# Kernel tuning notes

Measured on AMD Instinct MI355X. Metric: run time of the kernel, lower is better.

The kernel has to match this reference:

```python
import jax, jax.numpy as jnp
import numpy as np

B, S, E = 2, 2048, 1024
INNER = 2048          # proj_factor * embedding_dim
NH = 4                # mLSTM heads
K = 4                 # causal conv kernel size
PH, PD = 512, 4       # headwise-proj heads (inner/qkv_proj_blocksize) and block size


def setup_inputs() -> dict:
    key = jax.random.key(0)
    ks = jax.random.split(key, 10)
    f = lambda k, shape, s=0.02: jax.random.normal(k, shape, jnp.float32) * s
    return dict(
        x=jax.random.normal(ks[0], (B, S, E), jnp.float32),
        W_up=f(ks[1], (E, 2 * INNER)),
        conv_w=f(ks[2], (K, INNER), 0.1),
        conv_b=jnp.zeros((INNER,), jnp.float32),
        Wq=f(ks[3], (PH, PD, PD), 0.3),
        Wk=f(ks[4], (PH, PD, PD), 0.3),
        Wv=f(ks[5], (PH, PD, PD), 0.3),
        W_ig=f(ks[6], (3 * INNER, NH), 0.01),
        b_ig=jnp.zeros((NH,), jnp.float32),
        W_fg=f(ks[7], (3 * INNER, NH), 0.01),
        b_fg=jnp.linspace(3.0, 6.0, NH).astype(jnp.float32),
        norm_w=jnp.ones((INNER,), jnp.float32),
        skip=jnp.ones((INNER,), jnp.float32),
        W_down=f(ks[8], (INNER, E)),
    )


def _forward(x, W_up, conv_w, conv_b, Wq, Wk, Wv, W_ig, b_ig, W_fg, b_fg,
             norm_w, skip, W_down):
    Bx, Sx, _ = x.shape
    # up projection then split into mlstm branch and gate branch z
    x_inner = x @ W_up                                  # (B,S,2*INNER)
    x_mlstm, z = jnp.split(x_inner, 2, axis=-1)
    # causal depthwise conv1d (left-pad K-1)
    Kk = conv_w.shape[0]
    x_pad = jnp.pad(x_mlstm, ((0, 0), (Kk - 1, 0), (0, 0)))
    x_conv = sum(x_pad[:, i:i + Sx, :] * conv_w[i] for i in range(Kk)) + conv_b
    x_act = jax.nn.swish(x_conv)

    def headwise(t, W):
        H, o, d = W.shape
        return jnp.einsum('bshd,hod->bsho', t.reshape(Bx, Sx, H, d), W).reshape(Bx, Sx, H * o)

    q = headwise(x_act, Wq)
    k = headwise(x_act, Wk)
    v = headwise(x_mlstm, Wv)
    Dm = q.shape[-1]
    NHn = b_ig.shape[0]
    DH = Dm // NHn
    qh = q.reshape(Bx, Sx, NHn, DH).transpose(0, 2, 1, 3)   # (B,NH,S,DH)
    kh = k.reshape(Bx, Sx, NHn, DH).transpose(0, 2, 1, 3)
    vh = v.reshape(Bx, Sx, NHn, DH).transpose(0, 2, 1, 3)
    # input / forget gate preactivations from concat(q,k,v)
    if_in = jnp.concatenate([q, k, v], axis=-1)             # (B,S,3*INNER)
    ig = (if_in @ W_ig + b_ig).transpose(0, 2, 1)[..., None]  # (B,NH,S,1)
    fg = (if_in @ W_fg + b_fg).transpose(0, 2, 1)[..., None]
    # parallel stabilized mLSTM (matrix memory, exp gating)
    log_f = jax.nn.log_sigmoid(fg)
    lfc = jnp.concatenate([jnp.zeros((Bx, NHn, 1, 1), log_f.dtype),
                           jnp.cumsum(log_f, axis=2)], axis=2)  # (B,NH,S+1,1)
    lfm = lfc - jnp.swapaxes(lfc, -2, -1)                   # (B,NH,S+1,S+1)
    mask = jnp.tril(jnp.ones((Sx + 1, Sx + 1), bool))
    lfm = jnp.where(mask, lfm, -jnp.inf)[:, :, 1:, 1:]      # (B,NH,S,S)
    logD = lfm + jnp.swapaxes(ig, -2, -1)
    mD = jnp.max(logD, axis=-1, keepdims=True)
    Dmat = jnp.exp(logD - mD)
    C = jnp.einsum('bnsd,bntd->bnst', qh, kh) * (DH ** -0.5) * Dmat
    norm = jnp.maximum(jnp.abs(C.sum(-1, keepdims=True)), jnp.exp(-mD))
    h = jnp.einsum('bnst,bntd->bnsd', C / (norm + 1e-6), vh)  # (B,NH,S,DH)
    # multi-head layernorm over DH, then merge heads
    mu = h.mean(-1, keepdims=True)
    var = ((h - mu) ** 2).mean(-1, keepdims=True)
    hn = ((h - mu) * jax.lax.rsqrt(var + 1e-6)).transpose(0, 2, 1, 3).reshape(Bx, Sx, Dm)
    hn = hn * norm_w
    # learnable skip from conv activation, gate with swish(z), down proj
    h_state = (hn + skip * x_act) * jax.nn.swish(z)
    return h_state @ W_down


def reference(x, W_up, conv_w, conv_b, Wq, Wk, Wv, W_ig, b_ig, W_fg, b_fg,
              norm_w, skip, W_down):
    return _forward(x, W_up, conv_w, conv_b, Wq, Wk, Wv, W_ig, b_ig, W_fg,
                    b_fg, norm_w, skip, W_down)
```

## Files before the change

### kernel.cpp

```cpp
#include <hip/hip_runtime.h>
#include <math.h>

#define S_LEN 2048
#define INNERD 2048
#define NHEAD 4
#define DHEAD 512
#define BATCH 2
#define SCALE_QK 0.044194173824159216f

typedef __attribute__((ext_vector_type(8))) short short8v;
typedef __attribute__((ext_vector_type(4))) float f32x4;

#define MFMA_BF16(A, B, C) __builtin_amdgcn_mfma_f32_16x16x32_bf16(A, B, C, 0, 0, 0)

__device__ __forceinline__ void gll16(const void* g, void* l) {
  __builtin_amdgcn_global_load_lds((const __attribute__((address_space(1))) unsigned int*)g,
                                   (__attribute__((address_space(3))) unsigned int*)l,
                                   16, 0, 0);
}

__device__ __forceinline__ unsigned short f2bf(float x) {
  union { float f; unsigned u; } v; v.f = x;
  unsigned r = v.u + 0x7FFFu + ((v.u >> 16) & 1u);
  return (unsigned short)(r >> 16);
}
__device__ __forceinline__ float bf2f(unsigned short x) {
  union { unsigned u; float f; } v; v.u = ((unsigned)x) << 16; return v.f;
}
__device__ __forceinline__ float swishf(float x) { return x / (1.0f + __expf(-x)); }
__device__ __forceinline__ float logsigf(float x) {
  return (x >= 0.0f) ? -log1pf(expf(-x)) : (x - log1pf(expf(x)));
}

__global__ __launch_bounds__(256) void cast_kernel(const float* __restrict__ src,
                                                   unsigned short* __restrict__ dst) {
  const int i = (blockIdx.x * 256 + threadIdx.x) * 8;
  const float4 a = *(const float4*)(src + i);
  const float4 b = *(const float4*)(src + i + 4);
  short8v o;
  o[0] = (short)f2bf(a.x); o[1] = (short)f2bf(a.y); o[2] = (short)f2bf(a.z); o[3] = (short)f2bf(a.w);
  o[4] = (short)f2bf(b.x); o[5] = (short)f2bf(b.y); o[6] = (short)f2bf(b.z); o[7] = (short)f2bf(b.w);
  *(short8v*)(dst + i) = o;
}

__global__ __launch_bounds__(256) void trc_kernel(const float* __restrict__ src,
                                                  unsigned short* __restrict__ dst,
                                                  int R, int C) {
  const int t = threadIdx.x;
  const int r0 = blockIdx.y * 128, c0 = blockIdx.x * 128;
  const int rb = (t >> 4) * 8, cb2 = (t & 15) * 8;
  float vreg[8][8];
#pragma unroll
  for (int u = 0; u < 8; ++u) {
    const float4 p0 = *(const float4*)(src + (size_t)(r0 + rb + u) * C + c0 + cb2);
    const float4 p1 = *(const float4*)(src + (size_t)(r0 + rb + u) * C + c0 + cb2 + 4);
    vreg[u][0] = p0.x; vreg[u][1] = p0.y; vreg[u][2] = p0.z; vreg[u][3] = p0.w;
    vreg[u][4] = p1.x; vreg[u][5] = p1.y; vreg[u][6] = p1.z; vreg[u][7] = p1.w;
  }
#pragma unroll
  for (int j = 0; j < 8; ++j) {
    short8v o;
#pragma unroll
    for (int u = 0; u < 8; ++u) o[u] = (short)f2bf(vreg[u][j]);
    *(short8v*)(dst + (size_t)(c0 + cb2 + j) * R + r0 + rb) = o;
  }
}

__global__ __launch_bounds__(256) void trv_kernel(const unsigned short* __restrict__ v,
                                                  unsigned short* __restrict__ vt) {
  const int t = threadIdx.x;
  const int s0 = blockIdx.x * 128;
  const int d0 = blockIdx.y * 128;
  const int bn = blockIdx.z;
  const int b = bn >> 2, n = bn & 3;
  const int sb = (t >> 4) * 8, db = (t & 15) * 8;
  unsigned short r[8][8];
#pragma unroll
  for (int u = 0; u < 8; ++u) {
    const short8v x2 = *(const short8v*)(v + (size_t)(b * S_LEN + s0 + sb + u) * INNERD + n * DHEAD + d0 + db);
#pragma unroll
    for (int j = 0; j < 8; ++j) r[u][j] = (unsigned short)x2[j];
  }
#pragma unroll
  for (int j = 0; j < 8; ++j) {
    short8v o;
#pragma unroll
    for (int u = 0; u < 8; ++u) o[u] = (short)r[u][j];
    *(short8v*)(vt + (size_t)(bn * DHEAD + d0 + db + j) * S_LEN + s0 + sb) = o;
  }
}

__global__ __launch_bounds__(256) void prep_kernel(
    const float* __restrict__ Wq, const float* __restrict__ Wk, const float* __restrict__ Wv,
    const float* __restrict__ Wig, const float* __restrict__ Wfg,
    unsigned short* __restrict__ Wpk, unsigned short* __restrict__ CgT) {
  const int t = threadIdx.x;
  float wq[2][16], wk[2][16], wv[2][16];
#pragma unroll
  for (int hh = 0; hh < 2; ++hh) {
    const int h = 2 * t + hh;
#pragma unroll
    for (int j = 0; j < 16; ++j) {
      wq[hh][j] = Wq[(size_t)h * 16 + j];
      wk[hh][j] = Wk[(size_t)h * 16 + j];
      wv[hh][j] = Wv[(size_t)h * 16 + j];
    }
  }
#pragma unroll
  for (int hh = 0; hh < 2; ++hh)
#pragma unroll
    for (int sub = 0; sub < 2; ++sub) {
      short8v oq, ok, ov;
#pragma unroll
      for (int j = 0; j < 8; ++j) {
        oq[j] = (short)f2bf(wq[hh][sub * 8 + j]);
        ok[j] = (short)f2bf(wk[hh][sub * 8 + j]);
        ov[j] = (short)f2bf(wv[hh][sub * 8 + j]);
      }
      *(short8v*)(Wpk + ((size_t)(0 + hh * 2 + sub) * 256 + t) * 8) = oq;
      *(short8v*)(Wpk + ((size_t)(4 + hh * 2 + sub) * 256 + t) * 8) = ok;
      *(short8v*)(Wpk + ((size_t)(8 + hh * 2 + sub) * 256 + t) * 8) = ov;
    }
#pragma unroll
  for (int u = 0; u < 8; ++u) {
    const int hh = u >> 2, d = u & 3;
    const int h = 2 * t + hh;
    float cia[4] = {0, 0, 0, 0}, cim[4] = {0, 0, 0, 0};
    float cfa[4] = {0, 0, 0, 0}, cfm[4] = {0, 0, 0, 0};
#pragma unroll
    for (int o = 0; o < 4; ++o) {
      const int row = h * 4 + o;
      const float aq = wq[hh][o * 4 + d], ak = wk[hh][o * 4 + d], av = wv[hh][o * 4 + d];
#pragma unroll
      for (int g = 0; g < 4; ++g) {
        cia[g] += aq * Wig[(size_t)row * 4 + g] + ak * Wig[(size_t)(INNERD + row) * 4 + g];
        cim[g] += av * Wig[(size_t)(2 * INNERD + row) * 4 + g];
        cfa[g] += aq * Wfg[(size_t)row * 4 + g] + ak * Wfg[(size_t)(INNERD + row) * 4 + g];
        cfm[g] += av * Wfg[(size_t)(2 * INNERD + row) * 4 + g];
      }
    }
    const int c = t * 8 + u;
#pragma unroll
    for (int g = 0; g < 4; ++g) {
      CgT[(size_t)(g) * INNERD + c] = f2bf(cia[g]);
      CgT[(size_t)(4 + g) * INNERD + c] = f2bf(cim[g]);
      CgT[(size_t)(8 + g) * INNERD + c] = f2bf(cfa[g]);
      CgT[(size_t)(12 + g) * INNERD + c] = f2bf(cfm[g]);
    }
  }
}

template <int BN, int OUTMODE>
__global__ __launch_bounds__(256) void gemm_bf16(const unsigned short* __restrict__ A,
                                                 const unsigned short* __restrict__ Bt,
                                                 float* __restrict__ Cf,
                                                 unsigned short* __restrict__ Cb0,
                                                 unsigned short* __restrict__ Cb1,
                                                 int M, int N, int K) {
  constexpr int CB = BN / 32;
  __shared__ unsigned short As[128 * 64];
  __shared__ unsigned short Bs[BN * 64];
  const int tid = threadIdx.x;
  const int w = tid >> 6, l = tid & 63;
  const int lm = l & 15, l4 = l >> 4, l8 = l & 7, lr = l >> 3;
  const int nwg = gridDim.x * gridDim.y;
  int bid = blockIdx.y * gridDim.x + blockIdx.x;
  const int cpx = nwg >> 3;
  bid = (bid & 7) * cpx + (bid >> 3);
  const int bx = bid % gridDim.x, by = bid / gridDim.x;
  const int row0 = by * 128, col0 = bx * BN;
  const int wm = w >> 1, wn = w & 1;
  f32x4 acc[4 * CB];
#pragma unroll
  for (int i2 = 0; i2 < 4 * CB; ++i2) acc[i2] = (f32x4){0.f, 0.f, 0.f, 0.f};

  const int scol = (l8 * 16) ^ (lr << 4);

  for (int k0 = 0; k0 < K; k0 += 64) {
#pragma unroll
    for (int it = 0; it < 4; ++it) {
      const int r = it * 32 + w * 8 + lr;
      gll16((const char*)A + ((size_t)(row0 + r) * K + k0) * 2 + scol,
            (char*)As + (size_t)(it * 32 + w * 8) * 128);
    }
#pragma unroll
    for (int it = 0; it < BN / 32; ++it) {
      const int r = it * 32 + w * 8 + lr;
      gll16((const char*)Bt + ((size_t)(col0 + r) * K + k0) * 2 + scol,
            (char*)Bs + (size_t)(it * 32 + w * 8) * 128);
    }
    __syncthreads();
#pragma unroll
    for (int ks = 0; ks < 2; ++ks) {
      short8v af[4], bfr[CB];
#pragma unroll
      for (int rb = 0; rb < 4; ++rb) {
        const int row = wm * 64 + rb * 16 + lm;
        af[rb] = *(const short8v*)((const char*)As + row * 128 + ((ks * 64 + l4 * 16) ^ ((lm & 7) << 4)));
      }
#pragma unroll
      for (int cb = 0; cb < CB; ++cb) {
        const int row = wn * (BN / 2) + cb * 16 + lm;
        bfr[cb] = *(const short8v*)((const char*)Bs + row * 128 + ((ks * 64 + l4 * 16) ^ ((lm & 7) << 4)));
      }
      __builtin_amdgcn_s_setprio(1);
#pragma unroll
      for (int rb = 0; rb < 4; ++rb)
#pragma unroll
        for (int cb = 0; cb < CB; ++cb)
          acc[rb * CB + cb] = MFMA_BF16(af[rb], bfr[cb], acc[rb * CB + cb]);
      __builtin_amdgcn_s_setprio(0);
    }
    __syncthreads();
  }
#pragma unroll
  for (int rb = 0; rb < 4; ++rb)
#pragma unroll
    for (int cb = 0; cb < CB; ++cb)
#pragma unroll
      for (int r = 0; r < 4; ++r) {
        const int gr = row0 + wm * 64 + rb * 16 + l4 * 4 + r;
        const int gc = col0 + wn * (BN / 2) + cb * 16 + lm;
        const float vv = acc[rb * CB + cb][r];
        if (OUTMODE == 0) {
          Cf[(size_t)gr * N + gc] = vv;
        } else {
          if (gc < 2048) Cb0[(size_t)gr * 2048 + gc] = f2bf(vv);
          else Cb1[(size_t)gr * 2048 + gc - 2048] = f2bf(vv);
        }
      }
}

__global__ __launch_bounds__(256) void headwise_kernel(
    const unsigned short* __restrict__ xm,
    const unsigned short* __restrict__ Wpk, const unsigned short* __restrict__ CgT,
    const float* __restrict__ cw, const float* __restrict__ cbias,
    const float* __restrict__ big, const float* __restrict__ bfg,
    unsigned short* __restrict__ q, unsigned short* __restrict__ k,
    unsigned short* __restrict__ v,
    float* __restrict__ igpre, float* __restrict__ fgpre) {
  __shared__ float red2[4][8];
  const int bs = blockIdx.x, t = threadIdx.x;
  const int s = bs & (S_LEN - 1);
  const int c0 = t * 8;
  float xa8[8], xm8[8];
  {
    float accv[8];
    const float4 cb0 = *(const float4*)(cbias + c0);
    const float4 cb1 = *(const float4*)(cbias + c0 + 4);
    accv[0] = cb0.x; accv[1] = cb0.y; accv[2] = cb0.z; accv[3] = cb0.w;
    accv[4] = cb1.x; accv[5] = cb1.y; accv[6] = cb1.z; accv[7] = cb1.w;
#pragma unroll
    for (int i = 0; i < 4; ++i) {
      if (s - 3 + i >= 0) {
        const short8v xv = *(const short8v*)(xm + (size_t)(bs - 3 + i) * INNERD + c0);
        const float4 w0 = *(const float4*)(cw + i * INNERD + c0);
        const float4 w1 = *(const float4*)(cw + i * INNERD + c0 + 4);
        const float wv2[8] = {w0.x, w0.y, w0.z, w0.w, w1.x, w1.y, w1.z, w1.w};
#pragma unroll
        for (int u = 0; u < 8; ++u) accv[u] += bf2f((unsigned short)xv[u]) * wv2[u];
      }
    }
    const short8v xs = *(const short8v*)(xm + (size_t)bs * INNERD + c0);
#pragma unroll
    for (int u = 0; u < 8; ++u) { xm8[u] = bf2f((unsigned short)xs[u]); xa8[u] = swishf(accv[u]); }
  }
  short8v qo, ko, vo;
#pragma unroll
  for (int hh = 0; hh < 2; ++hh)
#pragma unroll
    for (int sub = 0; sub < 2; ++sub) {
      const short8v wq = *(const short8v*)(Wpk + ((size_t)(0 + hh * 2 + sub) * 256 + t) * 8);
      const short8v wk = *(const short8v*)(Wpk + ((size_t)(4 + hh * 2 + sub) * 256 + t) * 8);
      const short8v wv3 = *(const short8v*)(Wpk + ((size_t)(8 + hh * 2 + sub) * 256 + t) * 8);
      float ql = 0, qh = 0, kl = 0, kh2 = 0, vl = 0, vh = 0;
#pragma unroll
      for (int d = 0; d < 4; ++d) {
        const float xa = xa8[hh * 4 + d], xv2 = xm8[hh * 4 + d];
        ql += bf2f((unsigned short)wq[d]) * xa;
        qh += bf2f((unsigned short)wq[4 + d]) * xa;
        kl += bf2f((unsigned short)wk[d]) * xa;
        kh2 += bf2f((unsigned short)wk[4 + d]) * xa;
        vl += bf2f((unsigned short)wv3[d]) * xv2;
        vh += bf2f((unsigned short)wv3[4 + d]) * xv2;
      }
      qo[hh * 4 + sub * 2] = (short)f2bf(ql); qo[hh * 4 + sub * 2 + 1] = (short)f2bf(qh);
      ko[hh * 4 + sub * 2] = (short)f2bf(kl); ko[hh * 4 + sub * 2 + 1] = (short)f2bf(kh2);
      vo[hh * 4 + sub * 2] = (short)f2bf(vl); vo[hh * 4 + sub * 2 + 1] = (short)f2bf(vh);
    }
  *(short8v*)(q + (size_t)bs * INNERD + c0) = qo;
  *(short8v*)(k + (size_t)bs * INNERD + c0) = ko;
  *(short8v*)(v + (size_t)bs * INNERD + c0) = vo;
  float r8[8];
#pragma unroll
  for (int j = 0; j < 4; ++j) {
    const short8v ca = *(const short8v*)(CgT + (size_t)j * INNERD + c0);
    const short8v cm = *(const short8v*)(CgT + (size_t)(4 + j) * INNERD + c0);
    const short8v fa = *(const short8v*)(CgT + (size_t)(8 + j) * INNERD + c0);
    const short8v fm = *(const short8v*)(CgT + (size_t)(12 + j) * INNERD + c0);
    float si = 0.f, sf = 0.f;
#pragma unroll
    for (int u = 0; u < 8; ++u) {
      si += xa8[u] * bf2f((unsigned short)ca[u]) + xm8[u] * bf2f((unsigned short)cm[u]);
      sf += xa8[u] * bf2f((unsigned short)fa[u]) + xm8[u] * bf2f((unsigned short)fm[u]);
    }
    r8[j] = si; r8[4 + j] = sf;
  }
  const int l = t & 63;
  const bool b1 = (l & 1), b2 = (l & 2), b4 = (l & 4);
  float t4[4];
#pragma unroll
  for (int i = 0; i < 4; ++i) {
    const float send = b1 ? r8[i] : r8[i + 4];
    const float recv = __shfl_xor(send, 1, 64);
    t4[i] = (b1 ? r8[i + 4] : r8[i]) + recv;
  }
  float u2[2];
#pragma unroll
  for (int i = 0; i < 2; ++i) {
    const float send = b2 ? t4[i] : t4[i + 2];
    const float recv = __shfl_xor(send, 2, 64);
    u2[i] = (b2 ? t4[i + 2] : t4[i]) + recv;
  }
  float wsum;
  {
    const float send = b4 ? u2[0] : u2[1];
    const float recv = __shfl_xor(send, 4, 64);
    wsum = (b4 ? u2[1] : u2[0]) + recv;
  }
  wsum += __shfl_xor(wsum, 8, 64);
  wsum += __shfl_xor(wsum, 16, 64);
  wsum += __shfl_xor(wsum, 32, 64);
  if (l < 8) {
    const int perm = ((l & 1) << 2) | (l & 2) | ((l >> 2) & 1);
    red2[t >> 6][perm] = wsum;
  }
  __syncthreads();
  if (t < 8) {
    const float sum = red2[0][t] + red2[1][t] + red2[2][t] + red2[3][t];
    const int b = bs >> 11;
    if (t < 4) igpre[((size_t)(b * NHEAD + t)) * S_LEN + s] = sum + big[t];
    else fgpre[((size_t)(b * NHEAD + t - 4)) * S_LEN + s] = sum + bfg[t - 4];
  }
}

__global__ __launch_bounds__(256) void scan_kernel(const float* __restrict__ igpre,
                                                   const float* __restrict__ fgpre,
                                                   float* __restrict__ a_o,
                                                   float* __restrict__ rm_o,
                                                   float* __restrict__ e_o) {
  __shared__ float sd[256];
  const int bn = blockIdx.x, t = threadIdx.x;
  const size_t base = (size_t)bn * S_LEN + t * 8;
  float cs[8];
  float run = 0.0f;
#pragma unroll
  for (int u = 0; u < 8; ++u) { run += logsigf(fgpre[base + u]); cs[u] = run; }
  sd[t] = run;
  __syncthreads();
  for (int off = 1; off < 256; off <<= 1) {
    const float vv2 = (t >= off) ? sd[t - off] : 0.0f;
    __syncthreads();
    sd[t] += vv2;
    __syncthreads();
  }
  const float exs = (t > 0) ? sd[t - 1] : 0.0f;
  __syncthreads();
  float av[8], pm[8];
  float rmax = -INFINITY;
#pragma unroll
  for (int u = 0; u < 8; ++u) {
    const float L = exs + cs[u];
    cs[u] = L;
    av[u] = igpre[base + u] - L;
    rmax = fmaxf(rmax, av[u]);
    pm[u] = rmax;
  }
  sd[t] = rmax;
  __syncthreads();
  for (int off = 1; off < 256; off <<= 1) {
    const float vv2 = (t >= off) ? sd[t - off] : -INFINITY;
    __syncthreads();
    sd[t] = fmaxf(sd[t], vv2);
    __syncthreads();
  }
  const float exm = (t > 0) ? sd[t - 1] : -INFINITY;
#pragma unroll
  for (int u = 0; u < 8; ++u) {
    const float rmv = fmaxf(exm, pm[u]);
    a_o[base + u] = av[u];
    rm_o[base + u] = rmv;
    e_o[base + u] = expf(-(cs[u] + rmv));
  }
}

__global__ __launch_bounds__(512, 2) void mlstm_mfma(
    const unsigned short* __restrict__ qg, const unsigned short* __restrict__ kg,
    const unsigned short* __restrict__ vtg,
    const float* __restrict__ ag, const float* __restrict__ rmg,
    float* __restrict__ hraw, float* __restrict__ rsumg) {
  __shared__ unsigned short Ks[2][64 * 512];
  __shared__ unsigned short Ps[64 * 64];
  __shared__ float rsl[8][16];
  const int tid = threadIdx.x;
  const int w = tid >> 6, l = tid & 63;
  const int lm = l & 15, l4 = l >> 4;
  const int beta = blockIdx.x;
  const int bn = beta & 7;
  const int part = (beta >> 3) & 1;
  const int idx = beta >> 4;
  const int qi = (idx < 16) ? (31 - idx) : (idx - 16);
  const int i0 = qi << 6;
  const int b = bn >> 2, n = bn & 3;
  float* hp = hraw + (size_t)part * ((size_t)BATCH * S_LEN * INNERD);
  float* rp = rsumg + (size_t)part * ((size_t)BATCH * NHEAD * S_LEN);

  const int rA = ((w >> 1) << 4) + lm;
  short8v qf[16];
  {
    const unsigned short* qp = qg + (size_t)(b * S_LEN + i0 + rA) * INNERD + n * DHEAD + l4 * 8;
#pragma unroll
    for (int ks = 0; ks < 16; ++ks) qf[ks] = *(const short8v*)(qp + ks * 32);
  }
  const int rD = ((w >> 1) << 4) + (l4 << 2);
  float rm4[4];
#pragma unroll
  for (int r = 0; r < 4; ++r) rm4[r] = rmg[(size_t)bn * S_LEN + i0 + rD + r];
  const int cb0 = (w & 1) << 1;

  f32x4 acc[16];
#pragma unroll
  for (int i2 = 0; i2 < 16; ++i2) acc[i2] = (f32x4){0.f, 0.f, 0.f, 0.f};
  float rs4[4] = {0.f, 0.f, 0.f, 0.f};

  const int ntau = (qi + 2 - part) >> 1;
  __builtin_amdgcn_sched_barrier(0);
  if (ntau > 0) {
#pragma unroll
    for (int it = 0; it < 8; ++it) {
      const int row = it * 8 + w;
      gll16((const char*)kg + ((size_t)(b * S_LEN + part * 64 + row) * INNERD + n * DHEAD) * 2 + ((l * 16) ^ (w << 4)),
            (char*)Ks[0] + row * 1024);
    }
  }
  __builtin_amdgcn_sched_barrier(0);

  for (int tau = 0; tau < ntau; ++tau) {
    const int j0 = (part + 2 * tau) << 6;
    const int cur = tau & 1;
    short8v vf[8];
#pragma unroll
    for (int db = 0; db < 4; ++db)
#pragma unroll
      for (int ks = 0; ks < 2; ++ks)
        vf[db * 2 + ks] = *(const short8v*)(vtg + (size_t)(bn * DHEAD + w * 64 + db * 16 + lm) * S_LEN + j0 + ks * 32 + l4 * 8);
    const float a0 = ag[(size_t)bn * S_LEN + j0 + cb0 * 16 + lm];
    const float a1 = ag[(size_t)bn * S_LEN + j0 + cb0 * 16 + 16 + lm];
    __builtin_amdgcn_sched_barrier(0);
    const bool hasnext = (tau + 1 < ntau);
    if (hasnext) {
#pragma unroll
      for (int it = 0; it < 8; ++it) {
        const int row = it * 8 + w;
        gll16((const char*)kg + ((size_t)(b * S_LEN + j0 + 128 + row) * INNERD + n * DHEAD) * 2 + ((l * 16) ^ (w << 4)),
              (char*)Ks[cur ^ 1] + row * 1024);
      }
    }
    __builtin_amdgcn_sched_barrier(0);
    if (hasnext) { asm volatile("s_waitcnt vmcnt(18)" ::: "memory"); }
    else         { asm volatile("s_waitcnt vmcnt(10)" ::: "memory"); }
    __builtin_amdgcn_sched_barrier(0);
    __builtin_amdgcn_s_barrier();
    f32x4 s0 = (f32x4){0.f, 0.f, 0.f, 0.f}, s1 = (f32x4){0.f, 0.f, 0.f, 0.f};
    const char* kb0 = (const char*)Ks[cur] + (cb0 * 16 + lm) * 1024;
    const char* kb1 = (const char*)Ks[cur] + ((cb0 + 1) * 16 + lm) * 1024;
    __builtin_amdgcn_s_setprio(1);
#pragma unroll
    for (int ks = 0; ks < 16; ++ks) {
      const int off = (ks * 64 + l4 * 16) ^ ((lm & 7) << 4);
      const short8v b0 = *(const short8v*)(kb0 + off);
      const short8v b1 = *(const short8v*)(kb1 + off);
      s0 = MFMA_BF16(qf[ks], b0, s0);
      s1 = MFMA_BF16(qf[ks], b1, s1);
    }
    __builtin_amdgcn_s_setprio(0);
#pragma unroll
    for (int half = 0; half < 2; ++half) {
      const f32x4 sv = half ? s1 : s0;
      const float av = half ? a1 : a0;
      const int jl = (cb0 + half) * 16 + lm;
#pragma unroll
      for (int r = 0; r < 4; ++r) {
        const int il = rD + r;
        const float es = __expf(av - rm4[r]);
        const float p = (j0 + jl <= i0 + il) ? sv[r] * SCALE_QK * es : 0.0f;
        rs4[r] += p;
        *((unsigned short*)((char*)Ps + il * 128 + ((jl * 2) ^ ((il & 7) << 4)))) = f2bf(p);
      }
    }
    asm volatile("s_waitcnt lgkmcnt(0)" ::: "memory");
    __builtin_amdgcn_sched_barrier(0);
    __builtin_amdgcn_s_barrier();
#pragma unroll
    for (int ks = 0; ks < 2; ++ks) {
      short8v pa[4];
#pragma unroll
      for (int rb = 0; rb < 4; ++rb)
        pa[rb] = *(const short8v*)((const char*)Ps + (rb * 16 + lm) * 128 + ((ks * 64 + l4 * 16) ^ ((lm & 7) << 4)));
      __builtin_amdgcn_s_setprio(1);
#pragma unroll
      for (int rb = 0; rb < 4; ++rb)
#pragma unroll
        for (int db = 0; db < 4; ++db)
          acc[rb * 4 + db] = MFMA_BF16(pa[rb], vf[db * 2 + ks], acc[rb * 4 + db]);
      __builtin_amdgcn_s_setprio(0);
    }
  }
#pragma unroll
  for (int r = 0; r < 4; ++r) {
    float v2 = rs4[r];
    v2 += __shfl_xor(v2, 1, 64);
    v2 += __shfl_xor(v2, 2, 64);
    v2 += __shfl_xor(v2, 4, 64);
    v2 += __shfl_xor(v2, 8, 64);
    if (lm == 0) rsl[w][l4 * 4 + r] = v2;
  }
  asm volatile("s_waitcnt lgkmcnt(0)" ::: "memory");
  __builtin_amdgcn_s_barrier();
  if (tid < 64) {
    const int rblk = tid >> 4, rloc = tid & 15;
    rp[(size_t)bn * S_LEN + i0 + rblk * 16 + rloc] = rsl[rblk * 2][rloc] + rsl[rblk * 2 + 1][rloc];
  }
#pragma unroll
  for (int rb = 0; rb < 4; ++rb)
#pragma unroll
    for (int db = 0; db < 4; ++db) {
      float* dst = hp + (size_t)(b * S_LEN + i0 + rb * 16 + l4 * 4) * INNERD + n * DHEAD + w * 64 + db * 16 + lm;
#pragma unroll
      for (int r = 0; r < 4; ++r) dst[(size_t)r * INNERD] = acc[rb * 4 + db][r];
    }
}

__global__ __launch_bounds__(256) void mhln_kernel(
    const float* __restrict__ h, const unsigned short* __restrict__ xm,
    const unsigned short* __restrict__ zb,
    const float* __restrict__ cw, const float* __restrict__ cbias,
    const float* __restrict__ rsumg, const float* __restrict__ eg,
    const float* __restrict__ normw, const float* __restrict__ skip,
    unsigned short* __restrict__ hstate) {
  const int bs = blockIdx.x, t = threadIdx.x;
  const int bb = bs >> 11, s = bs & (S_LEN - 1);
  const int n = t >> 6, lane = t & 63;
  const int cp0 = n * DHEAD + lane * 8;
  const size_t hb = (size_t)bs * INNERD + cp0;
  const size_t HOFF = (size_t)BATCH * S_LEN * INNERD;
  const int bn = bb * NHEAD + n;
  const float rsv = rsumg[(size_t)bn * S_LEN + s] + rsumg[(size_t)BATCH * NHEAD * S_LEN + bn * S_LEN + s];
  const float ev = eg[(size_t)bn * S_LEN + s];
  const float inorm = 1.0f / (fmaxf(fabsf(rsv), ev) + 1e-6f);
  const float4 v0 = *(const float4*)(h + hb);
  const float4 v1 = *(const float4*)(h + hb + 4);
  const float4 u0 = *(const float4*)(h + HOFF + hb);
  const float4 u1 = *(const float4*)(h + HOFF + hb + 4);
  float vals[8] = {(v0.x + u0.x) * inorm, (v0.y + u0.y) * inorm, (v0.z + u0.z) * inorm,
                   (v0.w + u0.w) * inorm, (v1.x + u1.x) * inorm, (v1.y + u1.y) * inorm,
                   (v1.z + u1.z) * inorm, (v1.w + u1.w) * inorm};
  float sum = 0.0f;
#pragma unroll
  for (int u = 0; u < 8; ++u) sum += vals[u];
#pragma unroll
  for (int m = 32; m >= 1; m >>= 1) sum += __shfl_xor(sum, m, 64);
  const float mu = sum * (1.0f / 512.0f);
  float vs2 = 0.0f;
#pragma unroll
  for (int u = 0; u < 8; ++u) { const float d = vals[u] - mu; vs2 += d * d; }
#pragma unroll
  for (int m = 32; m >= 1; m >>= 1) vs2 += __shfl_xor(vs2, m, 64);
  const float rstd = rsqrtf(vs2 * (1.0f / 512.0f) + 1e-6f);
  float xa8[8];
  {
    float accv[8];
#pragma unroll
    for (int u = 0; u < 8; ++u) accv[u] = cbias[cp0 + u];
#pragma unroll
    for (int i2 = 0; i2 < 4; ++i2) {
      const int sj = s - 3 + i2;
      if (sj >= 0) {
        const short8v xv = *(const short8v*)(xm + (size_t)(bs - 3 + i2) * INNERD + cp0);
#pragma unroll
        for (int u = 0; u < 8; ++u)
          accv[u] += bf2f((unsigned short)xv[u]) * cw[i2 * INNERD + cp0 + u];
      }
    }
#pragma unroll
    for (int u = 0; u < 8; ++u) xa8[u] = swishf(accv[u]);
  }
  const short8v zv = *(const short8v*)(zb + (size_t)bs * INNERD + cp0);
  short8v o;
#pragma unroll
  for (int u = 0; u < 8; ++u) {
    const int cp = cp0 + u;
    const float hn = (vals[u] - mu) * rstd * normw[cp];
    const float z = bf2f((unsigned short)zv[u]);
    o[u] = (short)f2bf((hn + skip[cp] * xa8[u]) * swishf(z));
  }
  *(short8v*)(hstate + hb) = o;
}

extern "C" void kernel_launch(void* const* d_in, const int* in_sizes, int n_in,
                              void* d_out, int out_size, void* d_ws, size_t ws_size,
                              hipStream_t stream) {
  const float* x     = (const float*)d_in[0];
  const float* Wup   = (const float*)d_in[1];
  const float* cw    = (const float*)d_in[2];
  const float* cb    = (const float*)d_in[3];
  const float* Wq    = (const float*)d_in[4];
  const float* Wk    = (const float*)d_in[5];
  const float* Wv    = (const float*)d_in[6];
  const float* Wig   = (const float*)d_in[7];
  const float* big   = (const float*)d_in[8];
  const float* Wfg   = (const float*)d_in[9];
  const float* bfg   = (const float*)d_in[10];
  const float* normw = (const float*)d_in[11];
  const float* skip  = (const float*)d_in[12];
  const float* Wdown = (const float*)d_in[13];
  float* out = (float*)d_out;

  float* ws = (float*)d_ws;
  size_t off = 0;
  const size_t MR = (size_t)BATCH * S_LEN;
  const size_t GSZ = (size_t)BATCH * NHEAD * S_LEN;
  unsigned short* xm  = (unsigned short*)(ws + off); off += MR * INNERD / 2;
  unsigned short* zb  = (unsigned short*)(ws + off); off += MR * INNERD / 2;
  float* hraw         = ws + off;                    off += 2 * MR * INNERD;
  unsigned short* qb  = (unsigned short*)(ws + off); off += MR * INNERD / 2;
  unsigned short* kb  = (unsigned short*)(ws + off); off += MR * INNERD / 2;
  unsigned short* vt  = (unsigned short*)(ws + off); off += MR * INNERD / 2;
  float* igpre  = ws + off; off += GSZ;
  float* fgpre  = ws + off; off += GSZ;
  float* a_buf  = ws + off; off += GSZ;
  float* rm_buf = ws + off; off += GSZ;
  float* e_buf  = ws + off; off += GSZ;
  float* rsum   = ws + off; off += 2 * GSZ;
  unsigned short* Wpk = (unsigned short*)(ws + off); off += 12 * 256 * 8 / 2;
  unsigned short* CgT = (unsigned short*)(ws + off); off += 16 * (size_t)INNERD / 2;
  if (ws_size < off * sizeof(float)) return;

  unsigned short* vb     = (unsigned short*)hraw;
  unsigned short* x_bf   = (unsigned short*)(hraw + MR * INNERD);
  unsigned short* WupT   = vt;
  unsigned short* WdT    = kb;
  unsigned short* hstate = qb;

  prep_kernel<<<1, 256, 0, stream>>>(Wq, Wk, Wv, Wig, Wfg, Wpk, CgT);
  cast_kernel<<<2048, 256, 0, stream>>>(x, x_bf);
  trc_kernel<<<dim3(32, 8), 256, 0, stream>>>(Wup, WupT, 1024, 4096);
  gemm_bf16<128, 1><<<dim3(32, 32), 256, 0, stream>>>(x_bf, WupT, nullptr, xm, zb, 4096, 4096, 1024);
  headwise_kernel<<<4096, 256, 0, stream>>>(xm, Wpk, CgT, cw, cb, big, bfg,
                                            qb, kb, vb, igpre, fgpre);
  trv_kernel<<<dim3(16, 4, 8), 256, 0, stream>>>(vb, vt);
  scan_kernel<<<8, 256, 0, stream>>>(igpre, fgpre, a_buf, rm_buf, e_buf);
  mlstm_mfma<<<512, 512, 0, stream>>>(qb, kb, vt, a_buf, rm_buf, hraw, rsum);
  trc_kernel<<<dim3(8, 16), 256, 0, stream>>>(Wdown, WdT, 2048, 1024);
  mhln_kernel<<<4096, 256, 0, stream>>>(hraw, xm, zb, cw, cb, rsum, e_buf, normw, skip, hstate);
  gemm_bf16<64, 0><<<dim3(16, 32), 256, 0, stream>>>(hstate, WdT, out, nullptr, nullptr, 4096, 1024, 2048);
}
```

Measured before the change: 396.2 us.

## Read K fragments directly from global memory instead of LDS double buffer

Removes the double-buffered 128KB LDS staging of K tiles (async global-to-LDS loads, vmcnt waits and a per-iteration barrier), and has each wave load its K fragments straight from global/L2 into registers for the QK MFMA. The P tile is double-buffered in LDS so the first per-iteration barrier can be dropped without a write-after-read hazard. This cuts LDS use sharply, which may raise occupancy and remove sync, but each wave now issues uncoalesced 16-byte global loads with no prefetch, so latency is exposed and K data is re-read by multiple waves.

Measured after the change: 525.2 us. 1.33x slower.

```diff
diff --git a/kernel.cpp b/kernel.cpp
--- a/kernel.cpp
+++ b/kernel.cpp
@@ -399,8 +399,7 @@
     const unsigned short* __restrict__ vtg,
     const float* __restrict__ ag, const float* __restrict__ rmg,
     float* __restrict__ hraw, float* __restrict__ rsumg) {
-  __shared__ unsigned short Ks[2][64 * 512];
-  __shared__ unsigned short Ps[64 * 64];
+  __shared__ unsigned short Ps[2][64 * 64];
   __shared__ float rsl[8][16];
   const int tid = threadIdx.x;
   const int w = tid >> 6, l = tid & 63;
@@ -428,23 +427,15 @@
   for (int r = 0; r < 4; ++r) rm4[r] = rmg[(size_t)bn * S_LEN + i0 + rD + r];
   const int cb0 = (w & 1) << 1;
 
+  const unsigned short* kb0 = kg + (size_t)(b * S_LEN + cb0 * 16 + lm) * INNERD + n * DHEAD + l4 * 8;
+  const unsigned short* kb1 = kb0 + (size_t)16 * INNERD;
+
   f32x4 acc[16];
 #pragma unroll
   for (int i2 = 0; i2 < 16; ++i2) acc[i2] = (f32x4){0.f, 0.f, 0.f, 0.f};
   float rs4[4] = {0.f, 0.f, 0.f, 0.f};
 
   const int ntau = (qi + 2 - part) >> 1;
-  __builtin_amdgcn_sched_barrier(0);
-  if (ntau > 0) {
-#pragma unroll
-    for (int it = 0; it < 8; ++it) {
-      const int row = it * 8 + w;
-      gll16((const char*)kg + ((size_t)(b * S_LEN + part * 64 + row) * INNERD + n * DHEAD) * 2 + ((l * 16) ^ (w << 4)),
-            (char*)Ks[0] + row * 1024);
-    }
-  }
-  __builtin_amdgcn_sched_barrier(0);
-
   for (int tau = 0; tau < ntau; ++tau) {
     const int j0 = (part + 2 * tau) << 6;
     const int cur = tau & 1;
@@ -456,34 +447,16 @@
         vf[db * 2 + ks] = *(const short8v*)(vtg + (size_t)(bn * DHEAD + w * 64 + db * 16 + lm) * S_LEN + j0 + ks * 32 + l4 * 8);
     const float a0 = ag[(size_t)bn * S_LEN + j0 + cb0 * 16 + lm];
     const float a1 = ag[(size_t)bn * S_LEN + j0 + cb0 * 16 + 16 + lm];
-    __builtin_amdgcn_sched_barrier(0);
-    const bool hasnext = (tau + 1 < ntau);
-    if (hasnext) {
-#pragma unroll
-      for (int it = 0; it < 8; ++it) {
-        const int row = it * 8 + w;
-        gll16((const char*)kg + ((size_t)(b * S_LEN + j0 + 128 + row) * INNERD + n * DHEAD) * 2 + ((l * 16) ^ (w << 4)),
-              (char*)Ks[cur ^ 1] + row * 1024);
-      }
-    }
-    __builtin_amdgcn_sched_barrier(0);
-    if (hasnext) { asm volatile("s_waitcnt vmcnt(18)" ::: "memory"); }
-    else         { asm volatile("s_waitcnt vmcnt(10)" ::: "memory"); }
-    __builtin_amdgcn_sched_barrier(0);
-    __builtin_amdgcn_s_barrier();
+    const unsigned short* kp0 = kb0 + (size_t)j0 * INNERD;
+    const unsigned short* kp1 = kb1 + (size_t)j0 * INNERD;
     f32x4 s0 = (f32x4){0.f, 0.f, 0.f, 0.f}, s1 = (f32x4){0.f, 0.f, 0.f, 0.f};
-    const char* kb0 = (const char*)Ks[cur] + (cb0 * 16 + lm) * 1024;
-    const char* kb1 = (const char*)Ks[cur] + ((cb0 + 1) * 16 + lm) * 1024;
-    __builtin_amdgcn_s_setprio(1);
 #pragma unroll
     for (int ks = 0; ks < 16; ++ks) {
-      const int off = (ks * 64 + l4 * 16) ^ ((lm & 7) << 4);
-      const short8v b0 = *(const short8v*)(kb0 + off);
-      const short8v b1 = *(const short8v*)(kb1 + off);
-      s0 = MFMA_BF16(qf[ks], b0, s0);
-      s1 = MFMA_BF16(qf[ks], b1, s1);
-    }
-    __builtin_amdgcn_s_setprio(0);
+      const short8v k0 = *(const short8v*)(kp0 + ks * 32);
+      const short8v k1 = *(const short8v*)(kp1 + ks * 32);
+      s0 = MFMA_BF16(qf[ks], k0, s0);
+      s1 = MFMA_BF16(qf[ks], k1, s1);
+    }
 #pragma unroll
     for (int half = 0; half < 2; ++half) {
       const f32x4 sv = half ? s1 : s0;
@@ -495,7 +468,7 @@
         const float es = __expf(av - rm4[r]);
         const float p = (j0 + jl <= i0 + il) ? sv[r] * SCALE_QK * es : 0.0f;
         rs4[r] += p;
-        *((unsigned short*)((char*)Ps + il * 128 + ((jl * 2) ^ ((il & 7) << 4)))) = f2bf(p);
+        *((unsigned short*)((char*)Ps[cur] + il * 128 + ((jl * 2) ^ ((il & 7) << 4)))) = f2bf(p);
       }
     }
     asm volatile("s_waitcnt lgkmcnt(0)" ::: "memory");
@@ -506,7 +479,7 @@
       short8v pa[4];
 #pragma unroll
       for (int rb = 0; rb < 4; ++rb)
-        pa[rb] = *(const short8v*)((const char*)Ps + (rb * 16 + lm) * 128 + ((ks * 64 + l4 * 16) ^ ((lm & 7) << 4)));
+        pa[rb] = *(const short8v*)((const char*)Ps[cur] + (rb * 16 + lm) * 128 + ((ks * 64 + l4 * 16) ^ ((lm & 7) << 4)));
       __builtin_amdgcn_s_setprio(1);
 #pragma unroll
       for (int rb = 0; rb < 4; ++rb)
```

## Fuse setup kernels into one launch and store mLSTM partials as bf16

Applied to the files above, without the earlier changes.

Merges the input cast, both weight transposes and the gate-weight prep into a single setup kernel, removing several launches and moving the W_down transpose earlier. The mLSTM kernel now writes its two partial outputs in bf16 instead of fp32, halving write and read traffic into the layernorm kernel. It also removes the priority hints around the MFMA loop in the GEMM. The bf16 partials lose some precision before normalization, and workspace aliasing is reorganized.

After: 382.1 us. -3.5%, faster.

```diff
diff --git a/kernel.cpp b/kernel.cpp
--- a/kernel.cpp
+++ b/kernel.cpp
@@ -32,22 +32,9 @@
   return (x >= 0.0f) ? -log1pf(expf(-x)) : (x - log1pf(expf(x)));
 }
 
-__global__ __launch_bounds__(256) void cast_kernel(const float* __restrict__ src,
-                                                   unsigned short* __restrict__ dst) {
-  const int i = (blockIdx.x * 256 + threadIdx.x) * 8;
-  const float4 a = *(const float4*)(src + i);
-  const float4 b = *(const float4*)(src + i + 4);
-  short8v o;
-  o[0] = (short)f2bf(a.x); o[1] = (short)f2bf(a.y); o[2] = (short)f2bf(a.z); o[3] = (short)f2bf(a.w);
-  o[4] = (short)f2bf(b.x); o[5] = (short)f2bf(b.y); o[6] = (short)f2bf(b.z); o[7] = (short)f2bf(b.w);
-  *(short8v*)(dst + i) = o;
-}
-
-__global__ __launch_bounds__(256) void trc_kernel(const float* __restrict__ src,
-                                                  unsigned short* __restrict__ dst,
-                                                  int R, int C) {
-  const int t = threadIdx.x;
-  const int r0 = blockIdx.y * 128, c0 = blockIdx.x * 128;
+__device__ __forceinline__ void trc_body(const float* __restrict__ src,
+                                         unsigned short* __restrict__ dst,
+                                         int R, int C, int r0, int c0, int t) {
   const int rb = (t >> 4) * 8, cb2 = (t & 15) * 8;
   float vreg[8][8];
 #pragma unroll
@@ -63,6 +50,87 @@
 #pragma unroll
     for (int u = 0; u < 8; ++u) o[u] = (short)f2bf(vreg[u][j]);
     *(short8v*)(dst + (size_t)(c0 + cb2 + j) * R + r0 + rb) = o;
+  }
+}
+
+__global__ __launch_bounds__(256) void setup_kernel(
+    const float* __restrict__ x, const float* __restrict__ Wup,
+    const float* __restrict__ Wdown,
+    const float* __restrict__ Wq, const float* __restrict__ Wk, const float* __restrict__ Wv,
+    const float* __restrict__ Wig, const float* __restrict__ Wfg,
+    unsigned short* __restrict__ x_bf, unsigned short* __restrict__ WupT,
+    unsigned short* __restrict__ WdT,
+    unsigned short* __restrict__ Wpk, unsigned short* __restrict__ CgT) {
+  const int bid = blockIdx.x;
+  const int t = threadIdx.x;
+  if (bid < 2048) {
+    const int i = (bid * 256 + t) * 8;
+    const float4 a = *(const float4*)(x + i);
+    const float4 b = *(const float4*)(x + i + 4);
+    short8v o;
+    o[0] = (short)f2bf(a.x); o[1] = (short)f2bf(a.y); o[2] = (short)f2bf(a.z); o[3] = (short)f2bf(a.w);
+    o[4] = (short)f2bf(b.x); o[5] = (short)f2bf(b.y); o[6] = (short)f2bf(b.z); o[7] = (short)f2bf(b.w);
+    *(short8v*)(x_bf + i) = o;
+  } else if (bid < 2304) {
+    const int local = bid - 2048;
+    trc_body(Wup, WupT, 1024, 4096, (local >> 5) * 128, (local & 31) * 128, t);
+  } else if (bid < 2432) {
+    const int local = bid - 2304;
+    trc_body(Wdown, WdT, 2048, 1024, (local >> 3) * 128, (local & 7) * 128, t);
+  } else {
+    float wq[2][16], wk[2][16], wv[2][16];
+#pragma unroll
+    for (int hh = 0; hh < 2; ++hh) {
+      const int h = 2 * t + hh;
+#pragma unroll
+      for (int j = 0; j < 16; ++j) {
+        wq[hh][j] = Wq[(size_t)h * 16 + j];
+        wk[hh][j] = Wk[(size_t)h * 16 + j];
+        wv[hh][j] = Wv[(size_t)h * 16 + j];
+      }
+    }
+#pragma unroll
+    for (int hh = 0; hh < 2; ++hh)
+#pragma unroll
+      for (int sub = 0; sub < 2; ++sub) {
+        short8v oq, ok, ov;
+#pragma unroll
+        for (int j = 0; j < 8; ++j) {
+          oq[j] = (short)f2bf(wq[hh][sub * 8 + j]);
+          ok[j] = (short)f2bf(wk[hh][sub * 8 + j]);
+          ov[j] = (short)f2bf(wv[hh][sub * 8 + j]);
+        }
+        *(short8v*)(Wpk + ((size_t)(0 + hh * 2 + sub) * 256 + t) * 8) = oq;
+        *(short8v*)(Wpk + ((size_t)(4 + hh * 2 + sub) * 256 + t) * 8) = ok;
+        *(short8v*)(Wpk + ((size_t)(8 + hh * 2 + sub) * 256 + t) * 8) = ov;
+      }
+#pragma unroll
+    for (int u = 0; u < 8; ++u) {
+      const int hh = u >> 2, d = u & 3;
+      const int h = 2 * t + hh;
+      float cia[4] = {0, 0, 0, 0}, cim[4] = {0, 0, 0, 0};
+      float cfa[4] = {0, 0, 0, 0}, cfm[4] = {0, 0, 0, 0};
+#pragma unroll
+      for (int o = 0; o < 4; ++o) {
+        const int row = h * 4 + o;
+        const float aq = wq[hh][o * 4 + d], ak = wk[hh][o * 4 + d], av = wv[hh][o * 4 + d];
+#pragma unroll
+        for (int g = 0; g < 4; ++g) {
+          cia[g] += aq * Wig[(size_t)row * 4 + g] + ak * Wig[(size_t)(INNERD + row) * 4 + g];
+          cim[g] += av * Wig[(size_t)(2 * INNERD + row) * 4 + g];
+          cfa[g] += aq * Wfg[(size_t)row * 4 + g] + ak * Wfg[(size_t)(INNERD + row) * 4 + g];
+          cfm[g] += av * Wfg[(size_t)(2 * INNERD + row) * 4 + g];
+        }
+      }
+      const int c = t * 8 + u;
+#pragma unroll
+      for (int g = 0; g < 4; ++g) {
+        CgT[(size_t)(g) * INNERD + c] = f2bf(cia[g]);
+        CgT[(size_t)(4 + g) * INNERD + c] = f2bf(cim[g]);
+        CgT[(size_t)(8 + g) * INNERD + c] = f2bf(cfa[g]);
+        CgT[(size_t)(12 + g) * INNERD + c] = f2bf(cfm[g]);
+      }
+    }
   }
 }
 
@@ -87,66 +155,6 @@
 #pragma unroll
     for (int u = 0; u < 8; ++u) o[u] = (short)r[u][j];
     *(short8v*)(vt + (size_t)(bn * DHEAD + d0 + db + j) * S_LEN + s0 + sb) = o;
-  }
-}
-
-__global__ __launch_bounds__(256) void prep_kernel(
-    const float* __restrict__ Wq, const float* __restrict__ Wk, const float* __restrict__ Wv,
-    const float* __restrict__ Wig, const float* __restrict__ Wfg,
-    unsigned short* __restrict__ Wpk, unsigned short* __restrict__ CgT) {
-  const int t = threadIdx.x;
-  float wq[2][16], wk[2][16], wv[2][16];
-#pragma unroll
-  for (int hh = 0; hh < 2; ++hh) {
-    const int h = 2 * t + hh;
-#pragma unroll
-    for (int j = 0; j < 16; ++j) {
-      wq[hh][j] = Wq[(size_t)h * 16 + j];
-      wk[hh][j] = Wk[(size_t)h * 16 + j];
-      wv[hh][j] = Wv[(size_t)h * 16 + j];
-    }
-  }
-#pragma unroll
-  for (int hh = 0; hh < 2; ++hh)
-#pragma unroll
-    for (int sub = 0; sub < 2; ++sub) {
-      short8v oq, ok, ov;
-#pragma unroll
-      for (int j = 0; j < 8; ++j) {
-        oq[j] = (short)f2bf(wq[hh][sub * 8 + j]);
-        ok[j] = (short)f2bf(wk[hh][sub * 8 + j]);
-        ov[j] = (short)f2bf(wv[hh][sub * 8 + j]);
-      }
-      *(short8v*)(Wpk + ((size_t)(0 + hh * 2 + sub) * 256 + t) * 8) = oq;
-      *(short8v*)(Wpk + ((size_t)(4 + hh * 2 + sub) * 256 + t) * 8) = ok;
-      *(short8v*)(Wpk + ((size_t)(8 + hh * 2 + sub) * 256 + t) * 8) = ov;
-    }
-#pragma unroll
-  for (int u = 0; u < 8; ++u) {
-    const int hh = u >> 2, d = u & 3;
-    const int h = 2 * t + hh;
-    float cia[4] = {0, 0, 0, 0}, cim[4] = {0, 0, 0, 0};
-    float cfa[4] = {0, 0, 0, 0}, cfm[4] = {0, 0, 0, 0};
-#pragma unroll
-    for (int o = 0; o < 4; ++o) {
-      const int row = h * 4 + o;
-      const float aq = wq[hh][o * 4 + d], ak = wk[hh][o * 4 + d], av = wv[hh][o * 4 + d];
-#pragma unroll
-      for (int g = 0; g < 4; ++g) {
-        cia[g] += aq * Wig[(size_t)row * 4 + g] + ak * Wig[(size_t)(INNERD + row) * 4 + g];
-        cim[g] += av * Wig[(size_t)(2 * INNERD + row) * 4 + g];
-        cfa[g] += aq * Wfg[(size_t)row * 4 + g] + ak * Wfg[(size_t)(INNERD + row) * 4 + g];
-        cfm[g] += av * Wfg[(size_t)(2 * INNERD + row) * 4 + g];
-      }
-    }
-    const int c = t * 8 + u;
-#pragma unroll
-    for (int g = 0; g < 4; ++g) {
-      CgT[(size_t)(g) * INNERD + c] = f2bf(cia[g]);
-      CgT[(size_t)(4 + g) * INNERD + c] = f2bf(cim[g]);
-      CgT[(size_t)(8 + g) * INNERD + c] = f2bf(cfa[g]);
-      CgT[(size_t)(12 + g) * INNERD + c] = f2bf(cfm[g]);
-    }
   }
 }
 
@@ -203,13 +211,11 @@
         const int row = wn * (BN / 2) + cb * 16 + lm;
         bfr[cb] = *(const short8v*)((const char*)Bs + row * 128 + ((ks * 64 + l4 * 16) ^ ((lm & 7) << 4)));
       }
-      __builtin_amdgcn_s_setprio(1);
 #pragma unroll
       for (int rb = 0; rb < 4; ++rb)
 #pragma unroll
         for (int cb = 0; cb < CB; ++cb)
           acc[rb * CB + cb] = MFMA_BF16(af[rb], bfr[cb], acc[rb * CB + cb]);
-      __builtin_amdgcn_s_setprio(0);
     }
     __syncthreads();
   }
@@ -398,7 +404,7 @@
     const unsigned short* __restrict__ qg, const unsigned short* __restrict__ kg,
     const unsigned short* __restrict__ vtg,
     const float* __restrict__ ag, const float* __restrict__ rmg,
-    float* __restrict__ hraw, float* __restrict__ rsumg) {
+    unsigned short* __restrict__ hraw, float* __restrict__ rsumg) {
   __shared__ unsigned short Ks[2][64 * 512];
   __shared__ unsigned short Ps[64 * 64];
   __shared__ float rsl[8][16];
@@ -412,7 +418,7 @@
   const int qi = (idx < 16) ? (31 - idx) : (idx - 16);
   const int i0 = qi << 6;
   const int b = bn >> 2, n = bn & 3;
-  float* hp = hraw + (size_t)part * ((size_t)BATCH * S_LEN * INNERD);
+  unsigned short* hp = hraw + (size_t)part * ((size_t)BATCH * S_LEN * INNERD);
   float* rp = rsumg + (size_t)part * ((size_t)BATCH * NHEAD * S_LEN);
 
   const int rA = ((w >> 1) << 4) + lm;
@@ -535,14 +541,14 @@
   for (int rb = 0; rb < 4; ++rb)
 #pragma unroll
     for (int db = 0; db < 4; ++db) {
-      float* dst = hp + (size_t)(b * S_LEN + i0 + rb * 16 + l4 * 4) * INNERD + n * DHEAD + w * 64 + db * 16 + lm;
-#pragma unroll
-      for (int r = 0; r < 4; ++r) dst[(size_t)r * INNERD] = acc[rb * 4 + db][r];
+      unsigned short* dst = hp + (size_t)(b * S_LEN + i0 + rb * 16 + l4 * 4) * INNERD + n * DHEAD + w * 64 + db * 16 + lm;
+#pragma unroll
+      for (int r = 0; r < 4; ++r) dst[(size_t)r * INNERD] = f2bf(acc[rb * 4 + db][r]);
     }
 }
 
 __global__ __launch_bounds__(256) void mhln_kernel(
-    const float* __restrict__ h, const unsigned short* __restrict__ xm,
+    const unsigned short* __restrict__ h, const unsigned short* __restrict__ xm,
     const unsigned short* __restrict__ zb,
     const float* __restrict__ cw, const float* __restrict__ cbias,
     const float* __restrict__ rsumg, const float* __restrict__ eg,
@@ -558,13 +564,12 @@
   const float rsv = rsumg[(size_t)bn * S_LEN + s] + rsumg[(size_t)BATCH * NHEAD * S_LEN + bn * S_LEN + s];
   const float ev = eg[(size_t)bn * S_LEN + s];
   const float inorm = 1.0f / (fmaxf(fabsf(rsv), ev) + 1e-6f);
-  const float4 v0 = *(const float4*)(h + hb);
-  const float4 v1 = *(const float4*)(h + hb + 4);
-  const float4 u0 = *(const float4*)(h + HOFF + hb);
-  const float4 u1 = *(const float4*)(h + HOFF + hb + 4);
-  float vals[8] = {(v0.x + u0.x) * inorm, (v0.y + u0.y) * inorm, (v0.z + u0.z) * inorm,
-                   (v0.w + u0.w) * inorm, (v1.x + u1.x) * inorm, (v1.y + u1.y) * inorm,
-                   (v1.z + u1.z) * inorm, (v1.w + u1.w) * inorm};
+  const short8v h0 = *(const short8v*)(h + hb);
+  const short8v h1 = *(const short8v*)(h + HOFF + hb);
+  float vals[8];
+#pragma unroll
+  for (int u = 0; u < 8; ++u)
+    vals[u] = (bf2f((unsigned short)h0[u]) + bf2f((unsigned short)h1[u])) * inorm;
   float sum = 0.0f;
 #pragma unroll
   for (int u = 0; u < 8; ++u) sum += vals[u];
@@ -632,10 +637,11 @@
   const size_t GSZ = (size_t)BATCH * NHEAD * S_LEN;
   unsigned short* xm  = (unsigned short*)(ws + off); off += MR * INNERD / 2;
   unsigned short* zb  = (unsigned short*)(ws + off); off += MR * INNERD / 2;
-  float* hraw         = ws + off;                    off += 2 * MR * INNERD;
+  unsigned short* hraw = (unsigned short*)(ws + off); off += MR * INNERD;
   unsigned short* qb  = (unsigned short*)(ws + off); off += MR * INNERD / 2;
   unsigned short* kb  = (unsigned short*)(ws + off); off += MR * INNERD / 2;
   unsigned short* vt  = (unsigned short*)(ws + off); off += MR * INNERD / 2;
+  unsigned short* WdT = (unsigned short*)(ws + off); off += (size_t)2048 * 1024 / 2;
   float* igpre  = ws + off; off += GSZ;
   float* fgpre  = ws + off; off += GSZ;
   float* a_buf  = ws + off; off += GSZ;
@@ -646,22 +652,19 @@
   unsigned short* CgT = (unsigned short*)(ws + off); off += 16 * (size_t)INNERD / 2;
   if (ws_size < off * sizeof(float)) return;
 
-  unsigned short* vb     = (unsigned short*)hraw;
-  unsigned short* x_bf   = (unsigned short*)(hraw + MR * INNERD);
+  unsigned short* vb     = hraw;
+  unsigned short* x_bf   = hraw + MR * INNERD;
   unsigned short* WupT   = vt;
-  unsigned short* WdT    = kb;
   unsigned short* hstate = qb;
 
-  prep_kernel<<<1, 256, 0, stream>>>(Wq, Wk, Wv, Wig, Wfg, Wpk, CgT);
-  cast_kernel<<<2048, 256, 0, stream>>>(x, x_bf);
-  trc_kernel<<<dim3(32, 8), 256, 0, stream>>>(Wup, WupT, 1024, 4096);
+  setup_kernel<<<2433, 256, 0, stream>>>(x, Wup, Wdown, Wq, Wk, Wv, Wig, Wfg,
+                                         x_bf, WupT, WdT, Wpk, CgT);
   gemm_bf16<128, 1><<<dim3(32, 32), 256, 0, stream>>>(x_bf, WupT, nullptr, xm, zb, 4096, 4096, 1024);
   headwise_kernel<<<4096, 256, 0, stream>>>(xm, Wpk, CgT, cw, cb, big, bfg,
                                             qb, kb, vb, igpre, fgpre);
   trv_kernel<<<dim3(16, 4, 8), 256, 0, stream>>>(vb, vt);
   scan_kernel<<<8, 256, 0, stream>>>(igpre, fgpre, a_buf, rm_buf, e_buf);
   mlstm_mfma<<<512, 512, 0, stream>>>(qb, kb, vt, a_buf, rm_buf, hraw, rsum);
-  trc_kernel<<<dim3(8, 16), 256, 0, stream>>>(Wdown, WdT, 2048, 1024);
   mhln_kernel<<<4096, 256, 0, stream>>>(hraw, xm, zb, cw, cb, rsum, e_buf, normw, skip, hstate);
   gemm_bf16<64, 0><<<dim3(16, 32), 256, 0, stream>>>(hstate, WdT, out, nullptr, nullptr, 4096, 1024, 2048);
 }
```
